# Performance work log

Measured on AMD Instinct MI355X. Metric: run time of the kernel, lower is better.

## Reference

```python
import jax, jax.numpy as jnp
import numpy as np

MODEL_DIM = 1024
NUM_HEADS = 16
D_K = MODEL_DIM // NUM_HEADS  # 64
MAX_SEQ_LEN = 3200
B, T = 2, 2048
THETA_BASE = 10000.0


def setup_inputs() -> dict:
    key = jax.random.key(0)
    ks = jax.random.split(key, 5)
    scale = 1.0 / np.sqrt(MODEL_DIM)
    x = jax.random.normal(ks[0], (B, T, MODEL_DIM), dtype=jnp.float32)
    wq = jax.random.normal(ks[1], (MODEL_DIM, MODEL_DIM), dtype=jnp.float32) * scale
    wk = jax.random.normal(ks[2], (MODEL_DIM, MODEL_DIM), dtype=jnp.float32) * scale
    wv = jax.random.normal(ks[3], (MODEL_DIM, MODEL_DIM), dtype=jnp.float32) * scale
    wo = jax.random.normal(ks[4], (MODEL_DIM, MODEL_DIM), dtype=jnp.float32) * scale
    bq = jnp.zeros((MODEL_DIM,), jnp.float32)
    bk = jnp.zeros((MODEL_DIM,), jnp.float32)
    bv = jnp.zeros((MODEL_DIM,), jnp.float32)
    bo = jnp.zeros((MODEL_DIM,), jnp.float32)
    # RoPE tables, exactly as precompute_rotation_matrix: theta duplicated
    # adjacently ([t0,t0,t1,t1,...]).
    theta = THETA_BASE ** (jnp.arange(D_K // 2, dtype=jnp.float32) * (-2.0 / D_K))
    ang = jnp.outer(jnp.arange(MAX_SEQ_LEN, dtype=jnp.float32), theta)  # [L, d/2]
    ang = jnp.repeat(ang, 2, axis=-1)  # [L, d]
    return {
        "x": x, "wq": wq, "bq": bq, "wk": wk, "bk": bk,
        "wv": wv, "bv": bv, "wo": wo, "bo": bo,
        "cos": jnp.cos(ang), "sin": jnp.sin(ang),
    }


def reference(x, wq, bq, wk, bk, wv, bv, wo, bo, cos, sin):
    b, t, dm = x.shape
    h, d = NUM_HEADS, dm // NUM_HEADS

    # NOTE: original uses .view(b, h, t, d) directly on [b, t, h*d] (no
    # transpose) — a nonstandard head split we replicate faithfully.
    xq = (x @ wq.T + bq).reshape(b, h, t, d)
    xk = (x @ wk.T + bk).reshape(b, h, t, d)
    xv = (x @ wv.T + bv).reshape(b, h, t, d)

    def rot_half(q):
        # pairs are adjacent (2i, 2i+1): out[2i] = -q[2i+1], out[2i+1] = q[2i]
        q2 = q.reshape(b, h, t, d // 2, 2)
        return jnp.stack([-q2[..., 1], q2[..., 0]], axis=-1).reshape(b, h, t, d)

    # NOTE: original indexes cos/sin at the single position `seq_len`
    # (rotation_matrix_cos[:, :, xq.shape[2], :]), broadcasting one row over
    # all positions — replicated faithfully.
    c = cos[t]  # [d]
    s = sin[t]  # [d]
    xq = xq * c + rot_half(xq) * s
    xk = xk * c + rot_half(xk) * s

    scores = jnp.einsum("bhqd,bhkd->bhqk", xq, xk) / np.sqrt(d)
    p = jax.nn.softmax(scores, axis=-1)  # mask='none', dropout=0.0
    o = jnp.einsum("bhqk,bhkd->bhqd", p, xv)
    o = o.transpose(0, 2, 1, 3).reshape(b, t, dm)  # 'b h t d -> b t (h d)'
    return o @ wo.T + bo
```

## Files before the change

### kernel.cpp

```cpp
#include <hip/hip_runtime.h>

typedef _Float16 half8 __attribute__((ext_vector_type(8)));
typedef __fp16 pkh2 __attribute__((ext_vector_type(2)));
typedef float floatx4 __attribute__((ext_vector_type(4)));

#define AS1 __attribute__((address_space(1)))
#define AS3 __attribute__((address_space(3)))


__global__ __launch_bounds__(256) void convert_kernel(
    const float* __restrict__ x, const float* __restrict__ wq,
    const float* __restrict__ wk, const float* __restrict__ wv,
    const float* __restrict__ wo,
    _Float16* __restrict__ xb, _Float16* __restrict__ wqkv,
    _Float16* __restrict__ wob)
{
    int i = (blockIdx.x * 256 + threadIdx.x) * 4;
    const float* src; _Float16* dst; int off;
    if (i < 4194304)      { src = x;  dst = xb;            off = i; }
    else if (i < 5242880) { src = wq; dst = wqkv;          off = i - 4194304; }
    else if (i < 6291456) { src = wk; dst = wqkv + 1048576; off = i - 5242880; }
    else if (i < 7340032) { src = wv; dst = wqkv + 2097152; off = i - 6291456; }
    else                  { src = wo; dst = wob;           off = i - 7340032; }
    float4 v = *(const float4*)(src + off);
    union { uint2 u; pkh2 h[2]; } o;
    o.h[0] = __builtin_amdgcn_cvt_pkrtz(v.x, v.y);
    o.h[1] = __builtin_amdgcn_cvt_pkrtz(v.z, v.w);
    *(uint2*)(dst + off) = o.u;
}

template<bool QKV>
__global__ __launch_bounds__(256) void gemm_kernel(
    const _Float16* __restrict__ A, const _Float16* __restrict__ W,
    const float* __restrict__ b0, const float* __restrict__ b1,
    const float* __restrict__ b2,
    const float* __restrict__ cosr, const float* __restrict__ sinr,
    _Float16* __restrict__ O0, _Float16* __restrict__ O1,
    _Float16* __restrict__ O2, float* __restrict__ Of)
{
    __shared__ __align__(16) _Float16 As[128 * 64];
    __shared__ __align__(16) _Float16 Bs[128 * 64];
    const int tid  = threadIdx.x;
    const int lane = tid & 63, w = tid >> 6;
    const int lrow = lane & 15, quad = lane >> 4;
    const int wr = (w & 1) * 64, wc = (w >> 1) * 64;
    const int arow0 = blockIdx.x * 128;
    const int brow0 = blockIdx.y * 128;

    const int r8 = lane >> 3;
    const int gcol = ((lane & 7) ^ r8) * 8;

    floatx4 acc[4][4] = {};

    for (int kk = 0; kk < 1024; kk += 64) {
        __syncthreads();
        for (int u = 0; u < 4; u++) {
            const int row = w * 32 + u * 8;
            __builtin_amdgcn_global_load_lds(
                (const AS1 unsigned*)(const void*)(A + (size_t)(arow0 + row + r8) * 1024 + kk + gcol),
                (AS3 unsigned*)(void*)(As + row * 64), 16, 0, 0);
            __builtin_amdgcn_global_load_lds(
                (const AS1 unsigned*)(const void*)(W + (size_t)(brow0 + row + r8) * 1024 + kk + gcol),
                (AS3 unsigned*)(void*)(Bs + row * 64), 16, 0, 0);
        }
        __syncthreads();
        for (int ks = 0; ks < 2; ks++) {
            const int swz = ((ks * 4 + quad) ^ (lrow & 7)) * 8;
            half8 af[4], bf[4];
            for (int mt = 0; mt < 4; mt++)
                af[mt] = *(const half8*)&As[(wr + mt * 16 + lrow) * 64 + swz];
            for (int nt = 0; nt < 4; nt++)
                bf[nt] = *(const half8*)&Bs[(wc + nt * 16 + lrow) * 64 + swz];
            for (int mt = 0; mt < 4; mt++)
                for (int nt = 0; nt < 4; nt++)
                    acc[mt][nt] = __builtin_amdgcn_mfma_f32_16x16x32_f16(
                        af[mt], bf[nt], acc[mt][nt], 0, 0, 0);
        }
    }

    if (QKV) {
        const int seg = blockIdx.y >> 3;
        const float* bias = seg == 0 ? b0 : (seg == 1 ? b1 : b2);
        _Float16* out = seg == 0 ? O0 : (seg == 1 ? O1 : O2);
        const int nbase = (blockIdx.y & 7) * 128 + wc;
        for (int nt = 0; nt < 4; nt++) {
            const int n = nbase + nt * 16 + lrow;
            const float bv = bias[n];
            const int dj = n & 63;
            const float cv = cosr[dj], sv = sinr[dj];
            const bool odd = (n & 1) != 0;
            const int ns = (seg == 1)
                ? ((n & ~56) | ((((n >> 3) ^ (n >> 6)) & 7) << 3))
                : n;
            for (int mt = 0; mt < 4; mt++)
                for (int r = 0; r < 4; r++) {
                    float v = acc[mt][nt][r] + bv;
                    if (seg < 2) {
                        float p = __shfl_xor(v, 1, 64);
                        v = odd ? (v * cv + p * sv) : (v * cv - p * sv);
                    }
                    if (seg == 0) v *= 0.125f;
                    int row = arow0 + wr + mt * 16 + quad * 4 + r;
                    out[row * 1024 + ns] = (_Float16)v;
                }
        }
    } else {
        const int nbase = blockIdx.y * 128 + wc;
        for (int nt = 0; nt < 4; nt++) {
            const int n = nbase + nt * 16 + lrow;
            const float bv = b0[n];
            for (int mt = 0; mt < 4; mt++)
                for (int r = 0; r < 4; r++) {
                    int row = arow0 + wr + mt * 16 + quad * 4 + r;
                    Of[row * 1024 + n] = acc[mt][nt][r] + bv;
                }
        }
    }
}

__global__ __launch_bounds__(256) void vtrans_kernel(
    const _Float16* __restrict__ V, _Float16* __restrict__ VT)
{
    __shared__ __align__(16) _Float16 T[64][72];
    const int tid = threadIdx.x;
    const int kt = blockIdx.x;
    const int bh = blockIdx.y;
    const int bi = bh >> 4, hi = bh & 15;
    const _Float16* Vh = V + (size_t)(bi * 2048 + hi * 128) * 1024 + kt * 4096;
    const int srow = tid >> 3, sblk = tid & 7;
    union { uint4 u; _Float16 h[8]; } a, b;
    a.u = *(const uint4*)(Vh + (2 * srow) * 64 + sblk * 8);
    b.u = *(const uint4*)(Vh + (2 * srow + 1) * 64 + sblk * 8);
    for (int j = 0; j < 8; j++) {
        union { unsigned u; _Float16 h[2]; } pk;
        pk.h[0] = a.h[j]; pk.h[1] = b.h[j];
        *(unsigned*)&T[sblk * 8 + j][2 * srow] = pk.u;
    }
    __syncthreads();
    const int d = tid >> 2, c = tid & 3;
    const int xr = d & 7;
    _Float16* outrow = VT + ((size_t)bh * 64 + d) * 2048 + kt * 64;
    *(uint4*)(outrow + ((2 * c)     ^ xr) * 8) = *(const uint4*)&T[d][c * 16];
    *(uint4*)(outrow + ((2 * c + 1) ^ xr) * 8) = *(const uint4*)&T[d][c * 16 + 8];
}

__global__ __launch_bounds__(512, 4) void attn_kernel(
    const _Float16* __restrict__ Q, const _Float16* __restrict__ K,
    const _Float16* __restrict__ VT, _Float16* __restrict__ O)
{
    __shared__ __align__(16) _Float16 smem[26624];

    const int tid  = threadIdx.x;
    const int g    = tid >> 8;
    const int t8   = tid & 255;
    const int wg   = tid >> 6;
    const int w    = wg & 3;
    const int lane = tid & 63;
    const int lrow = lane & 15, quad = lane >> 4;

    const int bid = blockIdx.x;
    const int bh  = (bid & 7) * 4 + (bid >> 7);
    const int qt  = (bid >> 3) & 15;
    const int bi = bh >> 4, hi = bh & 15;
    const size_t base = (size_t)(bi * 2048 + hi * 128) * 1024;
    const _Float16* Qh  = Q + base;
    const _Float16* Kh  = K + base + (size_t)g * 65536;
    const _Float16* VTh = VT + (size_t)bh * 131072 + g * 1024;

    _Float16* Ksg  = smem + g * 4096;
    _Float16* Vtsg = smem + 8192 + g * 4096;
    _Float16* Ptw  = smem + 16384 + wg * 1280;

    half8 qf[2][2];
    for (int nt = 0; nt < 2; nt++)
        for (int ks = 0; ks < 2; ks++)
            qf[nt][ks] = *(const half8*)(Qh + (qt * 128 + w * 32 + nt * 16 + lrow) * 64
                                          + ks * 32 + quad * 8);

    floatx4 oacc[4][2] = {};
    float lsum0 = 0.0f, lsum1 = 0.0f;

    const int srow = t8 >> 3, sblk = t8 & 7;
    const int vd = t8 >> 2;
    const int vq0 = (2 * (t8 & 3)) ^ (vd & 7);
    const int vq1 = vq0 ^ 1;
    const _Float16* vrow = VTh + (size_t)vd * 2048;

    uint4 k0 = *(const uint4*)(Kh + srow * 64 + sblk * 8);
    uint4 k1 = *(const uint4*)(Kh + (srow + 32) * 64 + sblk * 8);
    uint4 v0 = *(const uint4*)(vrow + vq0 * 8);
    uint4 v1 = *(const uint4*)(vrow + vq1 * 8);

    const float LOG2E = 1.44269504f;
    const float OFF   = -8.65617025f;

    for (int ktl = 0; ktl < 16; ktl++) {
        __syncthreads();
        *(uint4*)&Ksg[srow * 64 + sblk * 8]        = k0;
        *(uint4*)&Ksg[(srow + 32) * 64 + sblk * 8] = k1;
        *(uint4*)&Vtsg[vd * 64 + vq0 * 8] = v0;
        *(uint4*)&Vtsg[vd * 64 + vq1 * 8] = v1;
        if (ktl < 15) {
            const _Float16* Kt = Kh + (ktl + 1) * 4096;
            k0 = *(const uint4*)(Kt + srow * 64 + sblk * 8);
            k1 = *(const uint4*)(Kt + (srow + 32) * 64 + sblk * 8);
            const _Float16* Vt = vrow + (ktl + 1) * 64;
            v0 = *(const uint4*)(Vt + vq0 * 8);
            v1 = *(const uint4*)(Vt + vq1 * 8);
        }
        __syncthreads();
        for (int h = 0; h < 2; h++) {
            for (int k2 = 0; k2 < 2; k2++) {
                const int kt4 = h * 2 + k2;
                floatx4 s0 = {}, s1 = {};
                for (int ks = 0; ks < 2; ks++) {
                    half8 af = *(const half8*)&Ksg[(kt4 * 16 + lrow) * 64
                                 + (((ks * 4 + quad) ^ (lrow & 7)) * 8)];
                    s0 = __builtin_amdgcn_mfma_f32_16x16x32_f16(af, qf[0][ks], s0, 0, 0, 0);
                    s1 = __builtin_amdgcn_mfma_f32_16x16x32_f16(af, qf[1][ks], s1, 0, 0, 0);
                }
                float p00 = __builtin_amdgcn_exp2f(fmaf(s0[0], LOG2E, OFF));
                float p01 = __builtin_amdgcn_exp2f(fmaf(s0[1], LOG2E, OFF));
                float p02 = __builtin_amdgcn_exp2f(fmaf(s0[2], LOG2E, OFF));
                float p03 = __builtin_amdgcn_exp2f(fmaf(s0[3], LOG2E, OFF));
                float p10 = __builtin_amdgcn_exp2f(fmaf(s1[0], LOG2E, OFF));
                float p11 = __builtin_amdgcn_exp2f(fmaf(s1[1], LOG2E, OFF));
                float p12 = __builtin_amdgcn_exp2f(fmaf(s1[2], LOG2E, OFF));
                float p13 = __builtin_amdgcn_exp2f(fmaf(s1[3], LOG2E, OFF));
                lsum0 += (p00 + p01) + (p02 + p03);
                lsum1 += (p10 + p11) + (p12 + p13);
                union { uint2 u; pkh2 h2[2]; } pk0, pk1;
                pk0.h2[0] = __builtin_amdgcn_cvt_pkrtz(p00, p01);
                pk0.h2[1] = __builtin_amdgcn_cvt_pkrtz(p02, p03);
                pk1.h2[0] = __builtin_amdgcn_cvt_pkrtz(p10, p11);
                pk1.h2[1] = __builtin_amdgcn_cvt_pkrtz(p12, p13);
                *(uint2*)&Ptw[lrow * 40 + k2 * 16 + quad * 4]        = pk0.u;
                *(uint2*)&Ptw[(16 + lrow) * 40 + k2 * 16 + quad * 4] = pk1.u;
            }
            half8 bf0 = *(const half8*)&Ptw[lrow * 40 + quad * 8];
            half8 bf1 = *(const half8*)&Ptw[(16 + lrow) * 40 + quad * 8];
            for (int dt = 0; dt < 4; dt++) {
                half8 av = *(const half8*)&Vtsg[(dt * 16 + lrow) * 64
                              + (((h * 4 + quad) ^ (lrow & 7)) * 8)];
                oacc[dt][0] = __builtin_amdgcn_mfma_f32_16x16x32_f16(av, bf0, oacc[dt][0], 0, 0, 0);
                oacc[dt][1] = __builtin_amdgcn_mfma_f32_16x16x32_f16(av, bf1, oacc[dt][1], 0, 0, 0);
            }
        }
    }
    __syncthreads();

    float* X = (float*)smem;
    float* L = (float*)(smem + 16384);
    if (g == 1) {
        for (int dt = 0; dt < 4; dt++)
            for (int nt = 0; nt < 2; nt++)
                *(floatx4*)&X[((dt * 2 + nt) * 256 + w * 64 + lane) * 4] = oacc[dt][nt];
        L[(w * 64 + lane) * 2]     = lsum0;
        L[(w * 64 + lane) * 2 + 1] = lsum1;
    }
    __syncthreads();
    if (g == 0) {
        for (int dt = 0; dt < 4; dt++)
            for (int nt = 0; nt < 2; nt++)
                oacc[dt][nt] += *(const floatx4*)&X[((dt * 2 + nt) * 256 + w * 64 + lane) * 4];
        lsum0 += L[(w * 64 + lane) * 2];
        lsum1 += L[(w * 64 + lane) * 2 + 1];
        lsum0 += __shfl_xor(lsum0, 16, 64); lsum0 += __shfl_xor(lsum0, 32, 64);
        lsum1 += __shfl_xor(lsum1, 16, 64); lsum1 += __shfl_xor(lsum1, 32, 64);
        const float inv0 = 1.0f / lsum0, inv1 = 1.0f / lsum1;
        _Float16* Es = smem + 17408 + w * 2304;
        for (int dt = 0; dt < 4; dt++) {
            union { uint2 u; pkh2 h2[2]; } a0, a1;
            a0.h2[0] = __builtin_amdgcn_cvt_pkrtz(oacc[dt][0][0] * inv0, oacc[dt][0][1] * inv0);
            a0.h2[1] = __builtin_amdgcn_cvt_pkrtz(oacc[dt][0][2] * inv0, oacc[dt][0][3] * inv0);
            a1.h2[0] = __builtin_amdgcn_cvt_pkrtz(oacc[dt][1][0] * inv1, oacc[dt][1][1] * inv1);
            a1.h2[1] = __builtin_amdgcn_cvt_pkrtz(oacc[dt][1][2] * inv1, oacc[dt][1][3] * inv1);
            *(uint2*)&Es[lrow * 72 + dt * 16 + quad * 4]        = a0.u;
            *(uint2*)&Es[(16 + lrow) * 72 + dt * 16 + quad * 4] = a1.u;
        }
        const int rw = lane >> 1, hf = lane & 1;
        const size_t orow = (size_t)(bi * 2048 + qt * 128 + w * 32 + rw) * 1024
                            + hi * 64 + hf * 32;
        for (int i = 0; i < 4; i++)
            *(uint4*)(O + orow + i * 8) = *(const uint4*)&Es[rw * 72 + hf * 32 + i * 8];
    }
}

extern "C" void kernel_launch(void* const* d_in, const int* in_sizes, int n_in,
                              void* d_out, int out_size, void* d_ws, size_t ws_size,
                              hipStream_t stream) {
    const float* x    = (const float*)d_in[0];
    const float* wq   = (const float*)d_in[1];
    const float* bq   = (const float*)d_in[2];
    const float* wk   = (const float*)d_in[3];
    const float* bk   = (const float*)d_in[4];
    const float* wv   = (const float*)d_in[5];
    const float* bv   = (const float*)d_in[6];
    const float* wo   = (const float*)d_in[7];
    const float* bo   = (const float*)d_in[8];
    const float* cosT = (const float*)d_in[9];
    const float* sinT = (const float*)d_in[10];

    _Float16* ws   = (_Float16*)d_ws;
    _Float16* xb   = ws;
    _Float16* wqkv = xb + 4194304;
    _Float16* wob  = wqkv + 3145728;
    _Float16* Qb   = wob + 1048576;
    _Float16* Kb   = Qb + 4194304;
    _Float16* Vb   = Kb + 4194304;
    _Float16* Ob   = Vb + 4194304;
    _Float16* VTb  = xb;

    convert_kernel<<<8192, 256, 0, stream>>>(x, wq, wk, wv, wo, xb, wqkv, wob);
    gemm_kernel<true><<<dim3(32, 24), 256, 0, stream>>>(
        xb, wqkv, bq, bk, bv, cosT + 2048 * 64, sinT + 2048 * 64,
        Qb, Kb, Vb, nullptr);
    vtrans_kernel<<<dim3(32, 32), 256, 0, stream>>>(Vb, VTb);
    attn_kernel<<<dim3(512), 512, 0, stream>>>(Qb, Kb, VTb, Ob);
    gemm_kernel<false><<<dim3(32, 8), 256, 0, stream>>>(
        Ob, wob, bo, nullptr, nullptr, nullptr, nullptr,
        nullptr, nullptr, nullptr, (float*)d_out);
}
```

Before: 214.4 us.

## Load K fragments directly from global and double-buffer V via LDS DMA

The attention kernel stops staging K through shared memory. Each wave now reads its K MFMA fragments straight from global memory, so the K swizzle in the QKV GEMM epilogue is removed. V tiles are double-buffered in LDS with global_load_lds, which drops one of the two barriers per iteration. Separately, the output projection GEMM is templated on BM and launched with 64-row tiles, doubling its block count for better CU occupancy. The trade-off is more redundant global and L2 reads of K across waves, and less reuse per tile in the output GEMM.

```diff
diff --git a/kernel.cpp b/kernel.cpp
--- a/kernel.cpp
+++ b/kernel.cpp
@@ -29,7 +29,7 @@
     *(uint2*)(dst + off) = o.u;
 }
 
-template<bool QKV>
+template<bool QKV, int BM>
 __global__ __launch_bounds__(256) void gemm_kernel(
     const _Float16* __restrict__ A, const _Float16* __restrict__ W,
     const float* __restrict__ b0, const float* __restrict__ b1,
@@ -38,40 +38,44 @@
     _Float16* __restrict__ O0, _Float16* __restrict__ O1,
     _Float16* __restrict__ O2, float* __restrict__ Of)
 {
-    __shared__ __align__(16) _Float16 As[128 * 64];
+    constexpr int MT = BM / 32;
+    __shared__ __align__(16) _Float16 As[BM * 64];
     __shared__ __align__(16) _Float16 Bs[128 * 64];
     const int tid  = threadIdx.x;
     const int lane = tid & 63, w = tid >> 6;
     const int lrow = lane & 15, quad = lane >> 4;
-    const int wr = (w & 1) * 64, wc = (w >> 1) * 64;
-    const int arow0 = blockIdx.x * 128;
+    const int wr = (w & 1) * (BM / 2), wc = (w >> 1) * 64;
+    const int arow0 = blockIdx.x * BM;
     const int brow0 = blockIdx.y * 128;
 
     const int r8 = lane >> 3;
     const int gcol = ((lane & 7) ^ r8) * 8;
 
-    floatx4 acc[4][4] = {};
+    floatx4 acc[MT][4] = {};
 
     for (int kk = 0; kk < 1024; kk += 64) {
         __syncthreads();
+        for (int u = 0; u < MT; u++) {
+            const int row = w * (8 * MT) + u * 8;
+            __builtin_amdgcn_global_load_lds(
+                (const AS1 unsigned*)(const void*)(A + (size_t)(arow0 + row + r8) * 1024 + kk + gcol),
+                (AS3 unsigned*)(void*)(As + row * 64), 16, 0, 0);
+        }
         for (int u = 0; u < 4; u++) {
             const int row = w * 32 + u * 8;
             __builtin_amdgcn_global_load_lds(
-                (const AS1 unsigned*)(const void*)(A + (size_t)(arow0 + row + r8) * 1024 + kk + gcol),
-                (AS3 unsigned*)(void*)(As + row * 64), 16, 0, 0);
-            __builtin_amdgcn_global_load_lds(
                 (const AS1 unsigned*)(const void*)(W + (size_t)(brow0 + row + r8) * 1024 + kk + gcol),
                 (AS3 unsigned*)(void*)(Bs + row * 64), 16, 0, 0);
         }
         __syncthreads();
         for (int ks = 0; ks < 2; ks++) {
             const int swz = ((ks * 4 + quad) ^ (lrow & 7)) * 8;
-            half8 af[4], bf[4];
-            for (int mt = 0; mt < 4; mt++)
+            half8 af[MT], bf[4];
+            for (int mt = 0; mt < MT; mt++)
                 af[mt] = *(const half8*)&As[(wr + mt * 16 + lrow) * 64 + swz];
             for (int nt = 0; nt < 4; nt++)
                 bf[nt] = *(const half8*)&Bs[(wc + nt * 16 + lrow) * 64 + swz];
-            for (int mt = 0; mt < 4; mt++)
+            for (int mt = 0; mt < MT; mt++)
                 for (int nt = 0; nt < 4; nt++)
                     acc[mt][nt] = __builtin_amdgcn_mfma_f32_16x16x32_f16(
                         af[mt], bf[nt], acc[mt][nt], 0, 0, 0);
@@ -89,10 +93,7 @@
             const int dj = n & 63;
             const float cv = cosr[dj], sv = sinr[dj];
             const bool odd = (n & 1) != 0;
-            const int ns = (seg == 1)
-                ? ((n & ~56) | ((((n >> 3) ^ (n >> 6)) & 7) << 3))
-                : n;
-            for (int mt = 0; mt < 4; mt++)
+            for (int mt = 0; mt < MT; mt++)
                 for (int r = 0; r < 4; r++) {
                     float v = acc[mt][nt][r] + bv;
                     if (seg < 2) {
@@ -101,7 +102,7 @@
                     }
                     if (seg == 0) v *= 0.125f;
                     int row = arow0 + wr + mt * 16 + quad * 4 + r;
-                    out[row * 1024 + ns] = (_Float16)v;
+                    out[row * 1024 + n] = (_Float16)v;
                 }
         }
     } else {
@@ -109,7 +110,7 @@
         for (int nt = 0; nt < 4; nt++) {
             const int n = nbase + nt * 16 + lrow;
             const float bv = b0[n];
-            for (int mt = 0; mt < 4; mt++)
+            for (int mt = 0; mt < MT; mt++)
                 for (int r = 0; r < 4; r++) {
                     int row = arow0 + wr + mt * 16 + quad * 4 + r;
                     Of[row * 1024 + n] = acc[mt][nt][r] + bv;
@@ -152,7 +153,6 @@
 
     const int tid  = threadIdx.x;
     const int g    = tid >> 8;
-    const int t8   = tid & 255;
     const int wg   = tid >> 6;
     const int w    = wg & 3;
     const int lane = tid & 63;
@@ -167,9 +167,8 @@
     const _Float16* Kh  = K + base + (size_t)g * 65536;
     const _Float16* VTh = VT + (size_t)bh * 131072 + g * 1024;
 
-    _Float16* Ksg  = smem + g * 4096;
-    _Float16* Vtsg = smem + 8192 + g * 4096;
-    _Float16* Ptw  = smem + 16384 + wg * 1280;
+    _Float16* Vb  = smem + g * 8192;
+    _Float16* Ptw = smem + 16384 + wg * 1280;
 
     half8 qf[2][2];
     for (int nt = 0; nt < 2; nt++)
@@ -180,44 +179,43 @@
     floatx4 oacc[4][2] = {};
     float lsum0 = 0.0f, lsum1 = 0.0f;
 
-    const int srow = t8 >> 3, sblk = t8 & 7;
-    const int vd = t8 >> 2;
-    const int vq0 = (2 * (t8 & 3)) ^ (vd & 7);
-    const int vq1 = vq0 ^ 1;
-    const _Float16* vrow = VTh + (size_t)vd * 2048;
-
-    uint4 k0 = *(const uint4*)(Kh + srow * 64 + sblk * 8);
-    uint4 k1 = *(const uint4*)(Kh + (srow + 32) * 64 + sblk * 8);
-    uint4 v0 = *(const uint4*)(vrow + vq0 * 8);
-    uint4 v1 = *(const uint4*)(vrow + vq1 * 8);
+    const _Float16* vsrc = VTh + (size_t)(w * 8 + (lane >> 3)) * 2048 + (lane & 7) * 8;
+    const _Float16* ksrc = Kh + lrow * 64 + quad * 8;
+
+    for (int i = 0; i < 2; i++)
+        __builtin_amdgcn_global_load_lds(
+            (const AS1 unsigned*)(const void*)(vsrc + i * 65536),
+            (AS3 unsigned*)(void*)(Vb + i * 2048 + w * 512), 16, 0, 0);
+    __syncthreads();
 
     const float LOG2E = 1.44269504f;
     const float OFF   = -8.65617025f;
 
-    for (int ktl = 0; ktl < 16; ktl++) {
-        __syncthreads();
-        *(uint4*)&Ksg[srow * 64 + sblk * 8]        = k0;
-        *(uint4*)&Ksg[(srow + 32) * 64 + sblk * 8] = k1;
-        *(uint4*)&Vtsg[vd * 64 + vq0 * 8] = v0;
-        *(uint4*)&Vtsg[vd * 64 + vq1 * 8] = v1;
-        if (ktl < 15) {
-            const _Float16* Kt = Kh + (ktl + 1) * 4096;
-            k0 = *(const uint4*)(Kt + srow * 64 + sblk * 8);
-            k1 = *(const uint4*)(Kt + (srow + 32) * 64 + sblk * 8);
-            const _Float16* Vt = vrow + (ktl + 1) * 64;
-            v0 = *(const uint4*)(Vt + vq0 * 8);
-            v1 = *(const uint4*)(Vt + vq1 * 8);
-        }
-        __syncthreads();
+    for (int kt = 0; kt < 16; kt++) {
+        const int cur = kt & 1;
+        half8 kf[4][2];
+        {
+            const _Float16* kb = ksrc + kt * 4096;
+            for (int kt4 = 0; kt4 < 4; kt4++)
+                for (int ks = 0; ks < 2; ks++)
+                    kf[kt4][ks] = *(const half8*)(kb + kt4 * 1024 + ks * 32);
+        }
+        if (kt < 15) {
+            const _Float16* vs = vsrc + (kt + 1) * 64;
+            _Float16* vd = Vb + (cur ^ 1) * 4096 + w * 512;
+            for (int i = 0; i < 2; i++)
+                __builtin_amdgcn_global_load_lds(
+                    (const AS1 unsigned*)(const void*)(vs + i * 65536),
+                    (AS3 unsigned*)(void*)(vd + i * 2048), 16, 0, 0);
+        }
+        const _Float16* Vc = Vb + cur * 4096;
         for (int h = 0; h < 2; h++) {
             for (int k2 = 0; k2 < 2; k2++) {
                 const int kt4 = h * 2 + k2;
                 floatx4 s0 = {}, s1 = {};
                 for (int ks = 0; ks < 2; ks++) {
-                    half8 af = *(const half8*)&Ksg[(kt4 * 16 + lrow) * 64
-                                 + (((ks * 4 + quad) ^ (lrow & 7)) * 8)];
-                    s0 = __builtin_amdgcn_mfma_f32_16x16x32_f16(af, qf[0][ks], s0, 0, 0, 0);
-                    s1 = __builtin_amdgcn_mfma_f32_16x16x32_f16(af, qf[1][ks], s1, 0, 0, 0);
+                    s0 = __builtin_amdgcn_mfma_f32_16x16x32_f16(kf[kt4][ks], qf[0][ks], s0, 0, 0, 0);
+                    s1 = __builtin_amdgcn_mfma_f32_16x16x32_f16(kf[kt4][ks], qf[1][ks], s1, 0, 0, 0);
                 }
                 float p00 = __builtin_amdgcn_exp2f(fmaf(s0[0], LOG2E, OFF));
                 float p01 = __builtin_amdgcn_exp2f(fmaf(s0[1], LOG2E, OFF));
@@ -240,14 +238,14 @@
             half8 bf0 = *(const half8*)&Ptw[lrow * 40 + quad * 8];
             half8 bf1 = *(const half8*)&Ptw[(16 + lrow) * 40 + quad * 8];
             for (int dt = 0; dt < 4; dt++) {
-                half8 av = *(const half8*)&Vtsg[(dt * 16 + lrow) * 64
+                half8 av = *(const half8*)&Vc[(dt * 16 + lrow) * 64
                               + (((h * 4 + quad) ^ (lrow & 7)) * 8)];
                 oacc[dt][0] = __builtin_amdgcn_mfma_f32_16x16x32_f16(av, bf0, oacc[dt][0], 0, 0, 0);
                 oacc[dt][1] = __builtin_amdgcn_mfma_f32_16x16x32_f16(av, bf1, oacc[dt][1], 0, 0, 0);
             }
         }
-    }
-    __syncthreads();
+        __syncthreads();
+    }
 
     float* X = (float*)smem;
     float* L = (float*)(smem + 16384);
@@ -312,12 +310,12 @@
     _Float16* VTb  = xb;
 
     convert_kernel<<<8192, 256, 0, stream>>>(x, wq, wk, wv, wo, xb, wqkv, wob);
-    gemm_kernel<true><<<dim3(32, 24), 256, 0, stream>>>(
+    gemm_kernel<true, 128><<<dim3(32, 24), 256, 0, stream>>>(
         xb, wqkv, bq, bk, bv, cosT + 2048 * 64, sinT + 2048 * 64,
         Qb, Kb, Vb, nullptr);
     vtrans_kernel<<<dim3(32, 32), 256, 0, stream>>>(Vb, VTb);
     attn_kernel<<<dim3(512), 512, 0, stream>>>(Qb, Kb, VTb, Ob);
-    gemm_kernel<false><<<dim3(32, 8), 256, 0, stream>>>(
+    gemm_kernel<false, 64><<<dim3(64, 8), 256, 0, stream>>>(
         Ob, wob, bo, nullptr, nullptr, nullptr, nullptr,
         nullptr, nullptr, nullptr, (float*)d_out);
 }
```

Result: slower. 229.6 us (+7.1%).

## Assemble attention P fragments with permlane swaps and shrink output GEMM tile

Applied to the files above, without the earlier changes.

In the attention kernel, the softmax probability tile is no longer written to shared memory and read back. It is rearranged in registers with permlane32/permlane16 swap intrinsics, which removes LDS traffic and its latency on the inner loop. Separately, the GEMM kernel gains a BM template parameter, and the output projection runs with 64-row tiles on a 64x8 grid, doubling its block count from 256 so the CUs are better filled. The permlane lane mapping must match the MFMA B-operand layout exactly, and the smaller tiles reuse each weight tile less.

```diff
diff --git a/kernel.cpp b/kernel.cpp
--- a/kernel.cpp
+++ b/kernel.cpp
@@ -29,7 +29,7 @@
     *(uint2*)(dst + off) = o.u;
 }
 
-template<bool QKV>
+template<bool QKV, int BM>
 __global__ __launch_bounds__(256) void gemm_kernel(
     const _Float16* __restrict__ A, const _Float16* __restrict__ W,
     const float* __restrict__ b0, const float* __restrict__ b1,
@@ -38,40 +38,44 @@
     _Float16* __restrict__ O0, _Float16* __restrict__ O1,
     _Float16* __restrict__ O2, float* __restrict__ Of)
 {
-    __shared__ __align__(16) _Float16 As[128 * 64];
+    constexpr int MT = BM / 32;
+    __shared__ __align__(16) _Float16 As[BM * 64];
     __shared__ __align__(16) _Float16 Bs[128 * 64];
     const int tid  = threadIdx.x;
     const int lane = tid & 63, w = tid >> 6;
     const int lrow = lane & 15, quad = lane >> 4;
-    const int wr = (w & 1) * 64, wc = (w >> 1) * 64;
-    const int arow0 = blockIdx.x * 128;
+    const int wr = (w & 1) * (BM / 2), wc = (w >> 1) * 64;
+    const int arow0 = blockIdx.x * BM;
     const int brow0 = blockIdx.y * 128;
 
     const int r8 = lane >> 3;
     const int gcol = ((lane & 7) ^ r8) * 8;
 
-    floatx4 acc[4][4] = {};
+    floatx4 acc[MT][4] = {};
 
     for (int kk = 0; kk < 1024; kk += 64) {
         __syncthreads();
+        for (int u = 0; u < MT; u++) {
+            const int row = w * (8 * MT) + u * 8;
+            __builtin_amdgcn_global_load_lds(
+                (const AS1 unsigned*)(const void*)(A + (size_t)(arow0 + row + r8) * 1024 + kk + gcol),
+                (AS3 unsigned*)(void*)(As + row * 64), 16, 0, 0);
+        }
         for (int u = 0; u < 4; u++) {
             const int row = w * 32 + u * 8;
             __builtin_amdgcn_global_load_lds(
-                (const AS1 unsigned*)(const void*)(A + (size_t)(arow0 + row + r8) * 1024 + kk + gcol),
-                (AS3 unsigned*)(void*)(As + row * 64), 16, 0, 0);
-            __builtin_amdgcn_global_load_lds(
                 (const AS1 unsigned*)(const void*)(W + (size_t)(brow0 + row + r8) * 1024 + kk + gcol),
                 (AS3 unsigned*)(void*)(Bs + row * 64), 16, 0, 0);
         }
         __syncthreads();
         for (int ks = 0; ks < 2; ks++) {
             const int swz = ((ks * 4 + quad) ^ (lrow & 7)) * 8;
-            half8 af[4], bf[4];
-            for (int mt = 0; mt < 4; mt++)
+            half8 af[MT], bf[4];
+            for (int mt = 0; mt < MT; mt++)
                 af[mt] = *(const half8*)&As[(wr + mt * 16 + lrow) * 64 + swz];
             for (int nt = 0; nt < 4; nt++)
                 bf[nt] = *(const half8*)&Bs[(wc + nt * 16 + lrow) * 64 + swz];
-            for (int mt = 0; mt < 4; mt++)
+            for (int mt = 0; mt < MT; mt++)
                 for (int nt = 0; nt < 4; nt++)
                     acc[mt][nt] = __builtin_amdgcn_mfma_f32_16x16x32_f16(
                         af[mt], bf[nt], acc[mt][nt], 0, 0, 0);
@@ -92,7 +96,7 @@
             const int ns = (seg == 1)
                 ? ((n & ~56) | ((((n >> 3) ^ (n >> 6)) & 7) << 3))
                 : n;
-            for (int mt = 0; mt < 4; mt++)
+            for (int mt = 0; mt < MT; mt++)
                 for (int r = 0; r < 4; r++) {
                     float v = acc[mt][nt][r] + bv;
                     if (seg < 2) {
@@ -109,7 +113,7 @@
         for (int nt = 0; nt < 4; nt++) {
             const int n = nbase + nt * 16 + lrow;
             const float bv = b0[n];
-            for (int mt = 0; mt < 4; mt++)
+            for (int mt = 0; mt < MT; mt++)
                 for (int r = 0; r < 4; r++) {
                     int row = arow0 + wr + mt * 16 + quad * 4 + r;
                     Of[row * 1024 + n] = acc[mt][nt][r] + bv;
@@ -144,6 +148,19 @@
     *(uint4*)(outrow + ((2 * c + 1) ^ xr) * 8) = *(const uint4*)&T[d][c * 16 + 8];
 }
 
+static __device__ __forceinline__ half8 assemble_p(uint2 a, uint2 b) {
+    auto s32x = __builtin_amdgcn_permlane32_swap(a.x, b.x, false, false);
+    auto s32y = __builtin_amdgcn_permlane32_swap(a.y, b.y, false, false);
+    auto s16x = __builtin_amdgcn_permlane16_swap(s32x[0], s32x[1], false, false);
+    auto s16y = __builtin_amdgcn_permlane16_swap(s32y[0], s32y[1], false, false);
+    union { uint4 u; half8 h; } r;
+    r.u.x = s16x[0];
+    r.u.y = s16y[0];
+    r.u.z = s16x[1];
+    r.u.w = s16y[1];
+    return r.h;
+}
+
 __global__ __launch_bounds__(512, 4) void attn_kernel(
     const _Float16* __restrict__ Q, const _Float16* __restrict__ K,
     const _Float16* __restrict__ VT, _Float16* __restrict__ O)
@@ -169,7 +186,6 @@
 
     _Float16* Ksg  = smem + g * 4096;
     _Float16* Vtsg = smem + 8192 + g * 4096;
-    _Float16* Ptw  = smem + 16384 + wg * 1280;
 
     half8 qf[2][2];
     for (int nt = 0; nt < 2; nt++)
@@ -210,6 +226,7 @@
         }
         __syncthreads();
         for (int h = 0; h < 2; h++) {
+            union { uint2 u; pkh2 h2[2]; } pA[2], pB[2];
             for (int k2 = 0; k2 < 2; k2++) {
                 const int kt4 = h * 2 + k2;
                 floatx4 s0 = {}, s1 = {};
@@ -229,16 +246,13 @@
                 float p13 = __builtin_amdgcn_exp2f(fmaf(s1[3], LOG2E, OFF));
                 lsum0 += (p00 + p01) + (p02 + p03);
                 lsum1 += (p10 + p11) + (p12 + p13);
-                union { uint2 u; pkh2 h2[2]; } pk0, pk1;
-                pk0.h2[0] = __builtin_amdgcn_cvt_pkrtz(p00, p01);
-                pk0.h2[1] = __builtin_amdgcn_cvt_pkrtz(p02, p03);
-                pk1.h2[0] = __builtin_amdgcn_cvt_pkrtz(p10, p11);
-                pk1.h2[1] = __builtin_amdgcn_cvt_pkrtz(p12, p13);
-                *(uint2*)&Ptw[lrow * 40 + k2 * 16 + quad * 4]        = pk0.u;
-                *(uint2*)&Ptw[(16 + lrow) * 40 + k2 * 16 + quad * 4] = pk1.u;
+                pA[k2].h2[0] = __builtin_amdgcn_cvt_pkrtz(p00, p01);
+                pA[k2].h2[1] = __builtin_amdgcn_cvt_pkrtz(p02, p03);
+                pB[k2].h2[0] = __builtin_amdgcn_cvt_pkrtz(p10, p11);
+                pB[k2].h2[1] = __builtin_amdgcn_cvt_pkrtz(p12, p13);
             }
-            half8 bf0 = *(const half8*)&Ptw[lrow * 40 + quad * 8];
-            half8 bf1 = *(const half8*)&Ptw[(16 + lrow) * 40 + quad * 8];
+            half8 bf0 = assemble_p(pA[0].u, pA[1].u);
+            half8 bf1 = assemble_p(pB[0].u, pB[1].u);
             for (int dt = 0; dt < 4; dt++) {
                 half8 av = *(const half8*)&Vtsg[(dt * 16 + lrow) * 64
                               + (((h * 4 + quad) ^ (lrow & 7)) * 8)];
@@ -312,12 +326,12 @@
     _Float16* VTb  = xb;
 
     convert_kernel<<<8192, 256, 0, stream>>>(x, wq, wk, wv, wo, xb, wqkv, wob);
-    gemm_kernel<true><<<dim3(32, 24), 256, 0, stream>>>(
+    gemm_kernel<true, 128><<<dim3(32, 24), 256, 0, stream>>>(
         xb, wqkv, bq, bk, bv, cosT + 2048 * 64, sinT + 2048 * 64,
         Qb, Kb, Vb, nullptr);
     vtrans_kernel<<<dim3(32, 32), 256, 0, stream>>>(Vb, VTb);
     attn_kernel<<<dim3(512), 512, 0, stream>>>(Qb, Kb, VTb, Ob);
-    gemm_kernel<false><<<dim3(32, 8), 256, 0, stream>>>(
+    gemm_kernel<false, 64><<<dim3(64, 8), 256, 0, stream>>>(
         Ob, wob, bo, nullptr, nullptr, nullptr, nullptr,
         nullptr, nullptr, nullptr, (float*)d_out);
 }
```

Result: faster. 207.1 us (-3.4%).
